# Kernel tuning notes

Hardware: AMD Instinct MI355X
Metric: run time of the kernel (lower is better)

The kernel has to match this reference:

```python
import jax, jax.numpy as jnp
import numpy as np

N = 50000; E = 200000; H = 128; L = 3; T = 2; FOUT = 64
G = 1000; NP = 3; ATOM_V = 64; BOND_V = 8
EPS = 1e-5
_DEG_HIST = np.array([0., 50000., 75000., 50000., 25000.])
# PyG PNAConv: avg_deg['log'] = sum(hist[d] * log(d+1)) / num_nodes
AVG_DEG_LOG = float((np.log(np.arange(5) + 1.0) * _DEG_HIST).sum() / _DEG_HIST.sum())


def _bn(v, g, b):
    # training-mode BatchNorm1d (biased variance), eps=1e-5
    mu = v.mean(0)
    var = ((v - mu) ** 2).mean(0)
    return (v - mu) * jax.lax.rsqrt(var + EPS) * g + b


def setup_inputs() -> dict:
    key = jax.random.key(0)
    ks = jax.random.split(key, 16)
    def nrm(k, shape, fan):
        return (jax.random.normal(k, shape, dtype=jnp.float32) / np.sqrt(fan)).astype(jnp.float32)
    return {
        'x': jax.random.randint(ks[0], (N, 9), 0, ATOM_V),
        'edge_index': jax.random.randint(ks[1], (2, E), 0, N),
        'batch': jnp.sort(jax.random.randint(ks[2], (N,), 0, G)),
        'edge_attr_idx': jax.random.randint(ks[3], (E, 3), 0, BOND_V),
        'atom_emb': nrm(ks[4], (9, ATOM_V, H), H),
        'bond_emb': nrm(ks[5], (3, BOND_V, H), H),
        'edge_W': nrm(ks[6], (L, H, H), H), 'edge_b': jnp.zeros((L, H), jnp.float32),
        'pre_W': nrm(ks[7], (L, T, 3 * H, H), 3 * H), 'pre_b': jnp.zeros((L, T, H), jnp.float32),
        'post_W': nrm(ks[8], (L, T, 13 * H, FOUT), 13 * H), 'post_b': jnp.zeros((L, T, FOUT), jnp.float32),
        'lin_W': nrm(ks[9], (L, H, H), H), 'lin_b': jnp.zeros((L, H), jnp.float32),
        'bn_g': jnp.ones((L, H), jnp.float32), 'bn_b': jnp.zeros((L, H), jnp.float32),
        'mlp_W': nrm(ks[10], (2, H, H), H), 'mlp_b': jnp.zeros((2, H), jnp.float32),
        'mlp_g': jnp.ones((2, H), jnp.float32), 'mlp_be': jnp.zeros((2, H), jnp.float32),
        'hW1': nrm(ks[11], (H, H // 2), H), 'hb1': jnp.zeros((H // 2,), jnp.float32),
        'hg1': jnp.ones((H // 2,), jnp.float32), 'hbe1': jnp.zeros((H // 2,), jnp.float32),
        'hW2': nrm(ks[12], (H // 2, H // 4), H // 2), 'hb2': jnp.zeros((H // 4,), jnp.float32),
        'hg2': jnp.ones((H // 4,), jnp.float32), 'hbe2': jnp.zeros((H // 4,), jnp.float32),
        'hW3': nrm(ks[13], (H // 4, NP), H // 4), 'hb3': jnp.zeros((NP,), jnp.float32),
    }


def reference(x, edge_index, batch, edge_attr_idx, atom_emb, bond_emb,
              edge_W, edge_b, pre_W, pre_b, post_W, post_b, lin_W, lin_b,
              bn_g, bn_b, mlp_W, mlp_b, mlp_g, mlp_be,
              hW1, hb1, hg1, hbe1, hW2, hb2, hg2, hbe2, hW3, hb3):
    # encoders: sum of per-feature embeddings (OGB Atom/Bond encoder)
    h = atom_emb[jnp.arange(9), x].sum(1)               # [N,H]
    e = bond_emb[jnp.arange(3), edge_attr_idx].sum(1)   # [E,H]
    src, dst = edge_index[0], edge_index[1]
    cnt = jax.ops.segment_sum(jnp.ones((E,), jnp.float32), dst, N)
    deg = jnp.maximum(cnt, 1.0)[:, None, None]          # clamp(1), as in PyG scalers
    amp = jnp.log(deg + 1.0) / AVG_DEG_LOG
    att = AVG_DEG_LOG / jnp.log(deg + 1.0)
    has = (cnt > 0)[:, None, None]
    for l in range(L):
        ea = e @ edge_W[l] + edge_b[l]                                  # [E,H]
        msg_in = jnp.concatenate([h[dst], h[src], ea], -1)              # [E,3H]
        m = jnp.einsum('ef,tfh->eth', msg_in, pre_W[l]) + pre_b[l]      # [E,T,H]
        s1 = jax.ops.segment_sum(m, dst, N)
        s2 = jax.ops.segment_sum(m * m, dst, N)
        mean = s1 / deg
        std = jnp.sqrt(jax.nn.relu(s2 / deg - mean * mean) + EPS)
        mn = jnp.where(has, jax.ops.segment_min(m, dst, N), 0.0)
        mx = jnp.where(has, jax.ops.segment_max(m, dst, N), 0.0)
        agg = jnp.concatenate([mean, mn, mx, std], -1)                  # [N,T,4H]
        scaled = jnp.concatenate([agg, agg * amp, agg * att], -1)       # [N,T,12H]
        upd = jnp.concatenate(
            [jnp.broadcast_to(h[:, None, :], (N, T, H)), scaled], -1)   # [N,T,13H]
        o = jnp.einsum('ntf,tfo->nto', upd, post_W[l]) + post_b[l]      # [N,T,FOUT]
        o = o.reshape(N, T * FOUT) @ lin_W[l] + lin_b[l]                # [N,H]
        h = jax.nn.relu(_bn(o, bn_g[l], bn_b[l]))
    g = jax.ops.segment_sum(h, batch, G)                                # [G,H]
    for i in range(2):
        g = jax.nn.relu(_bn(g @ mlp_W[i] + mlp_b[i], mlp_g[i], mlp_be[i]))
    g = jax.nn.relu(_bn(g @ hW1 + hb1, hg1, hbe1))
    g = jax.nn.relu(_bn(g @ hW2 + hb2, hg2, hbe2))
    return g @ hW3 + hb3                                                # [G,NP]
```

## Files before the change

### kernel.cpp

```cpp
#include <hip/hip_runtime.h>
#include <math.h>


#define NN 50000
#define NE 200000
#define HD 128
#define NG 1000
#define EPSV 1e-5f
#define ALOGC 1.1330197327247628f

#define AP 1288
#define OPF 132
#define ECAP 512
#define SCB 49

typedef __bf16 bf16x8 __attribute__((ext_vector_type(8)));
typedef float f32x4 __attribute__((ext_vector_type(4)));

__device__ __forceinline__ unsigned short f2bf(float f) {
    unsigned int u = __float_as_uint(f);
    unsigned int r = (u + 0x7FFFu + ((u >> 16) & 1u)) >> 16;
    return (unsigned short)r;
}
__device__ __forceinline__ float bf2f(unsigned short h) {
    return __uint_as_float((unsigned int)h << 16);
}

__global__ void k_fill(float* __restrict__ o, float v, int n) {
    int i = blockIdx.x * 256 + threadIdx.x;
    if (i < n) o[i] = v;
}

__global__ void k_zero(float* __restrict__ z, int n) {
    int i = blockIdx.x * 256 + threadIdx.x;
    if (i < n) z[i] = 0.f;
}

__global__ __launch_bounds__(256) void k_encode_nodes(
    const int* __restrict__ x, const float* __restrict__ aemb, float* __restrict__ h) {
    __shared__ int xi[8][9];
    int nb = blockIdx.x * 8;
    int tid = threadIdx.x;
    if (tid < 72) xi[tid / 9][tid % 9] = x[nb * 9 + tid];
    __syncthreads();
    int node = tid >> 5, c4 = (tid & 31) * 4;
    float4 acc = make_float4(0.f, 0.f, 0.f, 0.f);
#pragma unroll
    for (int f = 0; f < 9; ++f) {
        float4 e = *(const float4*)(aemb + (size_t)(f * 64 + xi[node][f]) * HD + c4);
        acc.x += e.x; acc.y += e.y; acc.z += e.z; acc.w += e.w;
    }
    *(float4*)(h + (size_t)(nb + node) * HD + c4) = acc;
}

__global__ void k_count(const int* __restrict__ dst, int* __restrict__ cnt) {
    int e = blockIdx.x * 256 + threadIdx.x;
    if (e < NE) atomicAdd(&cnt[dst[e]], 1);
}

__global__ __launch_bounds__(1024) void k_scanA(const int* __restrict__ cnt,
                                                int* __restrict__ sc, int* __restrict__ tot) {
    __shared__ int buf[1024];
    int tid = threadIdx.x;
    int i = blockIdx.x * 1024 + tid;
    int v = (i < NN) ? cnt[i] : 0;
    buf[tid] = v;
    __syncthreads();
    for (int s = 1; s < 1024; s <<= 1) {
        int t = (tid >= s) ? buf[tid - s] : 0;
        __syncthreads();
        buf[tid] += t;
        __syncthreads();
    }
    if (i < NN) sc[i] = buf[tid];
    if (tid == 1023) tot[blockIdx.x] = buf[1023];
}

__global__ void k_scanB(const int* __restrict__ tot, int* __restrict__ offb) {
    if (threadIdx.x == 0) {
        int run = 0;
        for (int b = 0; b < SCB; ++b) { offb[b] = run; run += tot[b]; }
    }
}

__global__ __launch_bounds__(1024) void k_scanC(
    const int* __restrict__ cnt, const int* __restrict__ sc, const int* __restrict__ offb,
    int* __restrict__ rowptr, float* __restrict__ ampv, float* __restrict__ attv) {
    int i = blockIdx.x * 1024 + threadIdx.x;
    if (i == 0) rowptr[0] = 0;
    if (i < NN) {
        rowptr[i + 1] = offb[blockIdx.x] + sc[i];
        int v = cnt[i];
        float dg = (float)(v > 0 ? v : 1);
        float lg = logf(dg + 1.0f);
        ampv[i] = lg / ALOGC;
        attv[i] = ALOGC / lg;
    }
}

__global__ void k_scatter(const int* __restrict__ dst, const int* __restrict__ rowptr,
                          int* __restrict__ fill, int* __restrict__ eperm) {
    int e = blockIdx.x * 256 + threadIdx.x;
    if (e < NE) {
        int d = dst[e];
        int pos = rowptr[d] + atomicAdd(&fill[d], 1);
        eperm[pos] = e;
    }
}

__global__ void k_eprep(const int* __restrict__ ei, const int* __restrict__ eai,
                        const int* __restrict__ eperm, int* __restrict__ precs) {
    int p = blockIdx.x * 256 + threadIdx.x;
    if (p < NE) {
        int e = eperm[p];
        int cidx = eai[e * 3] | (eai[e * 3 + 1] << 3) | (eai[e * 3 + 2] << 6);
        precs[p] = ei[e] | (cidx << 17);
    }
}

__global__ void k_fold(const float* __restrict__ edge_W, const float* __restrict__ edge_b,
                       const float* __restrict__ pre_W, const float* __restrict__ pre_b,
                       float* __restrict__ cW, float* __restrict__ tb) {
    int l = blockIdx.y;
    int k = blockIdx.x;
    int tj = threadIdx.x;
    int t = tj >> 7, j = tj & 127;
    const float* pw = pre_W + ((size_t)(l * 2 + t) * 384 + 256) * 128 + j;
    if (k < 128) {
        const float* ew = edge_W + ((size_t)l * 128 + k) * 128;
        float acc = 0.f;
        for (int i = 0; i < 128; ++i) acc += ew[i] * pw[i * 128];
        cW[((size_t)l * 128 + k) * 256 + tj] = acc;
    } else {
        const float* eb = edge_b + l * 128;
        float acc = pre_b[(l * 2 + t) * 128 + j];
        for (int i = 0; i < 128; ++i) acc += eb[i] * pw[i * 128];
        tb[l * 256 + tj] = acc;
    }
}

__global__ void k_bond(const float* __restrict__ bemb, const float* __restrict__ cW,
                       float* __restrict__ bondc) {
    int v = blockIdx.x, f = blockIdx.y, l = blockIdx.z;
    int tj = threadIdx.x;
    const float* src = bemb + (size_t)(f * 8 + v) * 128;
    const float* w = cW + (size_t)l * 128 * 256;
    float acc = 0.f;
    for (int i = 0; i < 128; ++i) acc += src[i] * w[i * 256 + tj];
    bondc[(((size_t)l * 3 + f) * 8 + v) * 256 + tj] = acc;
}

__global__ void k_bcomb(const float* __restrict__ bondc, unsigned short* __restrict__ bcomb) {
    int ci = blockIdx.x, l = blockIdx.y, tj = threadIdx.x;
    const float* base = bondc + (size_t)l * 3 * 8 * 256;
    float v = base[((0 * 8) + (ci & 7)) * 256 + tj]
            + base[((1 * 8) + ((ci >> 3) & 7)) * 256 + tj]
            + base[((2 * 8) + (ci >> 6)) * 256 + tj];
    bcomb[((size_t)l * 512 + ci) * 256 + tj] = f2bf(v);
}

__device__ __forceinline__ void pack_body2(const float* __restrict__ W, int N, int NT,
                                           unsigned short* __restrict__ pkh,
                                           unsigned short* __restrict__ pkl,
                                           int blk, int lane) {
    int kstep = blk / NT, nt = blk - kstep * NT;
    int kb = kstep * 32 + (lane >> 4) * 8;
    int col = nt * 16 + (lane & 15);
    unsigned short th[8], tl[8];
#pragma unroll
    for (int i = 0; i < 8; ++i) {
        float w = W[(size_t)(kb + i) * N + col];
        unsigned short hh = f2bf(w);
        th[i] = hh;
        tl[i] = f2bf(w - bf2f(hh));
    }
    size_t base = ((size_t)blk * 64 + lane) * 8;
    *(uint4*)(pkh + base) = *(uint4*)th;
    *(uint4*)(pkl + base) = *(uint4*)tl;
}

__global__ __launch_bounds__(64) void k_packall(
    const float* __restrict__ post_W, const float* __restrict__ lin_W,
    const float* __restrict__ pre_W,
    unsigned short* __restrict__ pkPostHi, unsigned short* __restrict__ pkPostLo,
    unsigned short* __restrict__ pkLinHi, unsigned short* __restrict__ pkLinLo,
    unsigned short* __restrict__ pkPreHi, unsigned short* __restrict__ pkPreLo) {
    int b = blockIdx.x;
    int lane = threadIdx.x;
    if (b < 1248) {
        int l = b / 416, rem = b % 416;
        int t = rem / 208, blk = rem % 208;
        size_t off = ((size_t)l * 2 + t) * 106496;
        pack_body2(post_W + ((size_t)l * 2 + t) * 1664 * 64, 64, 4,
                   pkPostHi + off, pkPostLo + off, blk, lane);
    } else if (b < 1344) {
        int idx = b - 1248;
        int l = idx / 32, blk = idx % 32;
        pack_body2(lin_W + (size_t)l * 128 * 128, 128, 8,
                   pkLinHi + (size_t)l * 16384, pkLinLo + (size_t)l * 16384, blk, lane);
    } else {
        int idx = b - 1344;
        int l = idx / 128, bb = idx % 128;
        const float* preW = pre_W + (size_t)l * 2 * 384 * 128;
        unsigned short* phi = pkPreHi + (size_t)l * 65536;
        unsigned short* plo = pkPreLo + (size_t)l * 65536;
        int kstep = bb >> 5, nt = bb & 31;
        int q = lane >> 4, nc = lane & 15;
        int col = nt * 16 + nc;
        int t = (col >> 7) & 1;
        int jcol = col & 127;
        int fbase = (col < 256) ? 0 : 128;
        unsigned short hi[8], lo[8];
#pragma unroll
        for (int i = 0; i < 8; ++i) {
            int k = kstep * 32 + q * 8 + i;
            float w = preW[((size_t)t * 384 + fbase + k) * 128 + jcol];
            unsigned short h16 = f2bf(w);
            hi[i] = h16;
            lo[i] = f2bf(w - bf2f(h16));
        }
        size_t base = ((size_t)bb * 64 + lane) * 8;
        *(uint4*)(phi + base) = *(uint4*)hi;
        *(uint4*)(plo + base) = *(uint4*)lo;
    }
}

__device__ __forceinline__ void pre_mfma_body(
    const unsigned short* __restrict__ ah, const unsigned short* __restrict__ al,
    const unsigned short* __restrict__ phi, const unsigned short* __restrict__ plo,
    const float* __restrict__ tb, int n0, int tid,
    float* __restrict__ hzd, unsigned short* __restrict__ hzs) {
    int lane = tid & 63, w = tid >> 6;
    int q = lane >> 4, nc = lane & 15;
    f32x4 acc[8];
#pragma unroll
    for (int j = 0; j < 8; ++j) acc[j] = (f32x4){0.f, 0.f, 0.f, 0.f};
#pragma unroll
    for (int kk = 0; kk < 4; ++kk) {
        bf16x8 Ahi = *(const bf16x8*)(ah + nc * 136 + kk * 32 + q * 8);
        bf16x8 Alo = *(const bf16x8*)(al + nc * 136 + kk * 32 + q * 8);
#pragma unroll
        for (int j = 0; j < 8; ++j) {
            int nt = w * 8 + j;
            size_t base = ((size_t)(kk * 32 + nt) * 64 + lane) * 8;
            bf16x8 Bhi = *(const bf16x8*)(phi + base);
            bf16x8 Blo = *(const bf16x8*)(plo + base);
            acc[j] = __builtin_amdgcn_mfma_f32_16x16x32_bf16(Ahi, Bhi, acc[j], 0, 0, 0);
            acc[j] = __builtin_amdgcn_mfma_f32_16x16x32_bf16(Ahi, Blo, acc[j], 0, 0, 0);
            acc[j] = __builtin_amdgcn_mfma_f32_16x16x32_bf16(Alo, Bhi, acc[j], 0, 0, 0);
        }
    }
#pragma unroll
    for (int j = 0; j < 8; ++j) {
        int col = (w * 8 + j) * 16 + nc;
#pragma unroll
        for (int reg = 0; reg < 4; ++reg) {
            int row = n0 + q * 4 + reg;
            if (col < 256) hzd[(size_t)row * 256 + col] = acc[j][reg] + tb[col];
            else           hzs[(size_t)row * 256 + (col - 256)] = f2bf(acc[j][reg]);
        }
    }
}

__global__ __launch_bounds__(256) void k_pre_m(
    const float* __restrict__ h,
    const unsigned short* __restrict__ phi, const unsigned short* __restrict__ plo,
    const float* __restrict__ tb,
    float* __restrict__ hzd, unsigned short* __restrict__ hzs) {
    __shared__ __align__(16) unsigned short ah[16 * 136];
    __shared__ __align__(16) unsigned short al[16 * 136];
    int n0 = blockIdx.x * 16;
    int tid = threadIdx.x;
    {
        int node = tid >> 4, cg = (tid & 15) * 8;
        const float* hs = h + (size_t)(n0 + node) * HD + cg;
        float4 v0 = *(const float4*)(hs);
        float4 v1 = *(const float4*)(hs + 4);
        float vv[8] = {v0.x, v0.y, v0.z, v0.w, v1.x, v1.y, v1.z, v1.w};
        unsigned short hh[8], ll[8];
#pragma unroll
        for (int i = 0; i < 8; ++i) {
            hh[i] = f2bf(vv[i]);
            ll[i] = f2bf(vv[i] - bf2f(hh[i]));
        }
        *(uint4*)(ah + node * 136 + cg) = *(uint4*)hh;
        *(uint4*)(al + node * 136 + cg) = *(uint4*)ll;
    }
    __syncthreads();
    pre_mfma_body(ah, al, phi, plo, tb, n0, tid, hzd, hzs);
}

__global__ __launch_bounds__(256) void k_bnpre(
    const float* __restrict__ o2, const float* __restrict__ stats,
    const float* __restrict__ g, const float* __restrict__ b,
    const unsigned short* __restrict__ phi, const unsigned short* __restrict__ plo,
    const float* __restrict__ tb,
    float* __restrict__ h, float* __restrict__ hzd, unsigned short* __restrict__ hzs) {
    __shared__ __align__(16) unsigned short ah[16 * 136];
    __shared__ __align__(16) unsigned short al[16 * 136];
    int n0 = blockIdx.x * 16;
    int tid = threadIdx.x;
    {
        int node = tid >> 4, cg = (tid & 15) * 8;
        int n = n0 + node;
        const float* os = o2 + (size_t)n * HD + cg;
        float4 v0 = *(const float4*)(os);
        float4 v1 = *(const float4*)(os + 4);
        float vv[8] = {v0.x, v0.y, v0.z, v0.w, v1.x, v1.y, v1.z, v1.w};
        unsigned short hh[8], ll[8];
        float ou[8];
#pragma unroll
        for (int i = 0; i < 8; ++i) {
            int c = cg + i;
            float mu = stats[c] * (1.f / NN);
            float var = stats[128 + c] * (1.f / NN) - mu * mu;
            float val = (vv[i] - mu) * rsqrtf(var + EPSV) * g[c] + b[c];
            val = fmaxf(val, 0.f);
            ou[i] = val;
            hh[i] = f2bf(val);
            ll[i] = f2bf(val - bf2f(hh[i]));
        }
        float* hd = h + (size_t)n * HD + cg;
        *(float4*)(hd) = make_float4(ou[0], ou[1], ou[2], ou[3]);
        *(float4*)(hd + 4) = make_float4(ou[4], ou[5], ou[6], ou[7]);
        *(uint4*)(ah + node * 136 + cg) = *(uint4*)hh;
        *(uint4*)(al + node * 136 + cg) = *(uint4*)ll;
    }
    __syncthreads();
    pre_mfma_body(ah, al, phi, plo, tb, n0, tid, hzd, hzs);
}

__global__ __launch_bounds__(256) void k_post(
    const float* __restrict__ h,
    const float* __restrict__ hzd, const unsigned short* __restrict__ hzs,
    const int* __restrict__ rowptr, const int* __restrict__ precs,
    const unsigned short* __restrict__ bcomb,
    const float* __restrict__ ampv, const float* __restrict__ attv,
    const unsigned short* __restrict__ pkPostHi, const unsigned short* __restrict__ pkPostLo,
    const float* __restrict__ postb,
    const unsigned short* __restrict__ pkLinHi, const unsigned short* __restrict__ pkLinLo,
    const float* __restrict__ linb,
    float* __restrict__ o2, float* __restrict__ stats) {
    __shared__ __align__(16) unsigned short a_lds[16 * AP];
    __shared__ __align__(16) float o_f[16 * OPF];
    __shared__ int es[ECAP];
    __shared__ float s_amp[16], s_att[16];
    int n0 = blockIdx.x * 16;
    int tid = threadIdx.x;

    int pbase = rowptr[n0];
    int ecount = rowptr[n0 + 16] - pbase;
    for (int i = tid; i < ecount && i < ECAP; i += 256) es[i] = precs[pbase + i];
    {
        int node = tid >> 4, cg = (tid & 15) * 8;
        const float* hs = h + (size_t)(n0 + node) * HD + cg;
        float4 v0 = *(const float4*)(hs);
        float4 v1 = *(const float4*)(hs + 4);
        unsigned short* d0 = a_lds + node * AP + cg;
        unsigned short* d1 = d0 + 640;
        unsigned short bb[8];
        bb[0] = f2bf(v0.x); bb[1] = f2bf(v0.y); bb[2] = f2bf(v0.z); bb[3] = f2bf(v0.w);
        bb[4] = f2bf(v1.x); bb[5] = f2bf(v1.y); bb[6] = f2bf(v1.z); bb[7] = f2bf(v1.w);
#pragma unroll
        for (int i = 0; i < 8; ++i) { d0[i] = bb[i]; d1[i] = bb[i]; }
    }
    if (tid < 16) { s_amp[tid] = ampv[n0 + tid]; s_att[tid] = attv[n0 + tid]; }
    __syncthreads();

    {
        int wv = tid >> 6, lane = tid & 63;
        int cc = lane * 4;
        int tt = cc >> 7, jj = cc & 127;
        bool incap = (ecount <= ECAP);
        const float4 Z4 = make_float4(0.f, 0.f, 0.f, 0.f);
        const float4 BIG = make_float4(3.4e38f, 3.4e38f, 3.4e38f, 3.4e38f);
        const float4 NBIG = make_float4(-3.4e38f, -3.4e38f, -3.4e38f, -3.4e38f);

#define EDGE_ACC(P, S1, S2, MN, MX)                                                       \
        {                                                                                 \
            int rec = incap ? es[(P) - pbase] : precs[(P)];                               \
            int sp = rec & 131071;                                                        \
            int ci = rec >> 17;                                                           \
            uint2 uv = *(const uint2*)(hzs + (size_t)sp * 256 + cc);                      \
            uint2 ub = *(const uint2*)(bcomb + (size_t)ci * 256 + cc);                    \
            float wx = __uint_as_float(uv.x << 16) + __uint_as_float(ub.x << 16);         \
            float wy = __uint_as_float(uv.x & 0xffff0000u) + __uint_as_float(ub.x & 0xffff0000u); \
            float wz = __uint_as_float(uv.y << 16) + __uint_as_float(ub.y << 16);         \
            float ww = __uint_as_float(uv.y & 0xffff0000u) + __uint_as_float(ub.y & 0xffff0000u); \
            S1.x += wx; S1.y += wy; S1.z += wz; S1.w += ww;                               \
            S2.x += wx * wx; S2.y += wy * wy; S2.z += wz * wz; S2.w += ww * ww;           \
            MN.x = fminf(MN.x, wx); MN.y = fminf(MN.y, wy);                               \
            MN.z = fminf(MN.z, wz); MN.w = fminf(MN.w, ww);                               \
            MX.x = fmaxf(MX.x, wx); MX.y = fmaxf(MX.y, wy);                               \
            MX.z = fmaxf(MX.z, wz); MX.w = fmaxf(MX.w, ww);                               \
        }

        auto fin = [&](int r, int cnt, float4 hd, float4 s1, float4 s2, float4 mn, float4 mx) {
            float inv = 1.f / (float)(cnt > 0 ? cnt : 1);
            float4 mw, stdv, mean;
            mw.x = s1.x * inv; mw.y = s1.y * inv; mw.z = s1.z * inv; mw.w = s1.w * inv;
            stdv.x = sqrtf(fmaxf(s2.x * inv - mw.x * mw.x, 0.f) + EPSV);
            stdv.y = sqrtf(fmaxf(s2.y * inv - mw.y * mw.y, 0.f) + EPSV);
            stdv.z = sqrtf(fmaxf(s2.z * inv - mw.z * mw.z, 0.f) + EPSV);
            stdv.w = sqrtf(fmaxf(s2.w * inv - mw.w * mw.w, 0.f) + EPSV);
            if (cnt > 0) {
                mean.x = hd.x + mw.x; mean.y = hd.y + mw.y;
                mean.z = hd.z + mw.z; mean.w = hd.w + mw.w;
                mn.x += hd.x; mn.y += hd.y; mn.z += hd.z; mn.w += hd.w;
                mx.x += hd.x; mx.y += hd.y; mx.z += hd.z; mx.w += hd.w;
            } else {
                mean = Z4; mn = Z4; mx = Z4;
            }
            unsigned short* d = a_lds + r * AP + tt * 640 + 128 + jj;
            d[0] = f2bf(mean.x); d[1] = f2bf(mean.y); d[2] = f2bf(mean.z); d[3] = f2bf(mean.w);
            d += 128; d[0] = f2bf(mn.x); d[1] = f2bf(mn.y); d[2] = f2bf(mn.z); d[3] = f2bf(mn.w);
            d += 128; d[0] = f2bf(mx.x); d[1] = f2bf(mx.y); d[2] = f2bf(mx.z); d[3] = f2bf(mx.w);
            d += 128; d[0] = f2bf(stdv.x); d[1] = f2bf(stdv.y); d[2] = f2bf(stdv.z); d[3] = f2bf(stdv.w);
        };

        for (int i = 0; i < 2; ++i) {
            int ra = wv * 4 + i * 2;
            int rb = ra + 1;
            int na = n0 + ra, nb = n0 + rb;
            int pa0 = rowptr[na], pa1 = rowptr[na + 1];
            int pb0 = rowptr[nb], pb1 = rowptr[nb + 1];
            float4 hda = *(const float4*)(hzd + (size_t)na * 256 + cc);
            float4 hdb = *(const float4*)(hzd + (size_t)nb * 256 + cc);
            float4 s1a = Z4, s2a = Z4, mna = BIG, mxa = NBIG;
            float4 s1b = Z4, s2b = Z4, mnb = BIG, mxb = NBIG;
            int da = pa1 - pa0, db = pb1 - pb0;
            int mc = (da < db) ? da : db;
            for (int k = 0; k < mc; ++k) {
                EDGE_ACC(pa0 + k, s1a, s2a, mna, mxa)
                EDGE_ACC(pb0 + k, s1b, s2b, mnb, mxb)
            }
            for (int k = mc; k < da; ++k) EDGE_ACC(pa0 + k, s1a, s2a, mna, mxa)
            for (int k = mc; k < db; ++k) EDGE_ACC(pb0 + k, s1b, s2b, mnb, mxb)
            fin(ra, da, hda, s1a, s2a, mna, mxa);
            fin(rb, db, hdb, s1b, s2b, mnb, mxb);
        }
#undef EDGE_ACC
    }
    __syncthreads();

    {
        int lane = tid & 63;
        int w = tid >> 6;
        int t = w >> 1;
        int ntb = (w & 1) * 2;
        int q = lane >> 4, nc = lane & 15;
        const unsigned short* arow = a_lds + (size_t)nc * AP + t * 640 + q * 8;
        size_t toff = (size_t)t * 106496;
        const unsigned short* pkh = pkPostHi + toff;
        const unsigned short* pkl = pkPostLo + toff;
        f32x4 aP0 = {0.f, 0.f, 0.f, 0.f}, aP1 = {0.f, 0.f, 0.f, 0.f};
        f32x4 aA0 = {0.f, 0.f, 0.f, 0.f}, aA1 = {0.f, 0.f, 0.f, 0.f};
        f32x4 aT0 = {0.f, 0.f, 0.f, 0.f}, aT1 = {0.f, 0.f, 0.f, 0.f};
        for (int kk = 0; kk < 20; ++kk) {
            bf16x8 af = *(const bf16x8*)(arow + kk * 32);
            size_t ib = ((size_t)(kk * 4 + ntb) * 64 + lane) * 8;
            aP0 = __builtin_amdgcn_mfma_f32_16x16x32_bf16(af, *(const bf16x8*)(pkh + ib), aP0, 0, 0, 0);
            aP0 = __builtin_amdgcn_mfma_f32_16x16x32_bf16(af, *(const bf16x8*)(pkl + ib), aP0, 0, 0, 0);
            aP1 = __builtin_amdgcn_mfma_f32_16x16x32_bf16(af, *(const bf16x8*)(pkh + ib + 512), aP1, 0, 0, 0);
            aP1 = __builtin_amdgcn_mfma_f32_16x16x32_bf16(af, *(const bf16x8*)(pkl + ib + 512), aP1, 0, 0, 0);
            if (kk >= 4) {
                size_t ia = ((size_t)((kk + 16) * 4 + ntb) * 64 + lane) * 8;
                aA0 = __builtin_amdgcn_mfma_f32_16x16x32_bf16(af, *(const bf16x8*)(pkh + ia), aA0, 0, 0, 0);
                aA0 = __builtin_amdgcn_mfma_f32_16x16x32_bf16(af, *(const bf16x8*)(pkl + ia), aA0, 0, 0, 0);
                aA1 = __builtin_amdgcn_mfma_f32_16x16x32_bf16(af, *(const bf16x8*)(pkh + ia + 512), aA1, 0, 0, 0);
                aA1 = __builtin_amdgcn_mfma_f32_16x16x32_bf16(af, *(const bf16x8*)(pkl + ia + 512), aA1, 0, 0, 0);
                size_t it = ((size_t)((kk + 32) * 4 + ntb) * 64 + lane) * 8;
                aT0 = __builtin_amdgcn_mfma_f32_16x16x32_bf16(af, *(const bf16x8*)(pkh + it), aT0, 0, 0, 0);
                aT0 = __builtin_amdgcn_mfma_f32_16x16x32_bf16(af, *(const bf16x8*)(pkl + it), aT0, 0, 0, 0);
                aT1 = __builtin_amdgcn_mfma_f32_16x16x32_bf16(af, *(const bf16x8*)(pkh + it + 512), aT1, 0, 0, 0);
                aT1 = __builtin_amdgcn_mfma_f32_16x16x32_bf16(af, *(const bf16x8*)(pkl + it + 512), aT1, 0, 0, 0);
            }
        }
#pragma unroll
        for (int u = 0; u < 2; ++u) {
            int nt = ntb + u;
            int col = t * 64 + nt * 16 + nc;
            float pbia = postb[t * 64 + nt * 16 + nc];
            f32x4 P = u ? aP1 : aP0;
            f32x4 A = u ? aA1 : aA0;
            f32x4 T = u ? aT1 : aT0;
#pragma unroll
            for (int reg = 0; reg < 4; ++reg) {
                int mrow = q * 4 + reg;
                o_f[mrow * OPF + col] = P[reg] + s_amp[mrow] * A[reg] + s_att[mrow] * T[reg] + pbia;
            }
        }
    }
    __syncthreads();

    {
        int lane = tid & 63;
        int w = tid >> 6;
        int ntb = w * 2;
        int q = lane >> 4, nc = lane & 15;
        const float* arow = o_f + (size_t)nc * OPF + q * 8;
        f32x4 L0 = {0.f, 0.f, 0.f, 0.f}, L1 = {0.f, 0.f, 0.f, 0.f};
#pragma unroll
        for (int kk = 0; kk < 4; ++kk) {
            float4 a0 = *(const float4*)(arow + kk * 32);
            float4 a1 = *(const float4*)(arow + kk * 32 + 4);
            float vv[8] = {a0.x, a0.y, a0.z, a0.w, a1.x, a1.y, a1.z, a1.w};
            unsigned short hh[8], ll[8];
#pragma unroll
            for (int i = 0; i < 8; ++i) {
                hh[i] = f2bf(vv[i]);
                ll[i] = f2bf(vv[i] - bf2f(hh[i]));
            }
            bf16x8 Ahi = *(const bf16x8*)hh;
            bf16x8 Alo = *(const bf16x8*)ll;
            size_t ib = ((size_t)(kk * 8 + ntb) * 64 + lane) * 8;
            bf16x8 B0h = *(const bf16x8*)(pkLinHi + ib);
            bf16x8 B0l = *(const bf16x8*)(pkLinLo + ib);
            bf16x8 B1h = *(const bf16x8*)(pkLinHi + ib + 512);
            bf16x8 B1l = *(const bf16x8*)(pkLinLo + ib + 512);
            L0 = __builtin_amdgcn_mfma_f32_16x16x32_bf16(Ahi, B0h, L0, 0, 0, 0);
            L0 = __builtin_amdgcn_mfma_f32_16x16x32_bf16(Alo, B0h, L0, 0, 0, 0);
            L0 = __builtin_amdgcn_mfma_f32_16x16x32_bf16(Ahi, B0l, L0, 0, 0, 0);
            L1 = __builtin_amdgcn_mfma_f32_16x16x32_bf16(Ahi, B1h, L1, 0, 0, 0);
            L1 = __builtin_amdgcn_mfma_f32_16x16x32_bf16(Alo, B1h, L1, 0, 0, 0);
            L1 = __builtin_amdgcn_mfma_f32_16x16x32_bf16(Ahi, B1l, L1, 0, 0, 0);
        }
#pragma unroll
        for (int u = 0; u < 2; ++u) {
            int col = (ntb + u) * 16 + nc;
            float lb = linb[col];
            f32x4 L = u ? L1 : L0;
            float ps = 0.f, pss = 0.f;
#pragma unroll
            for (int reg = 0; reg < 4; ++reg) {
                int mrow = q * 4 + reg;
                float v = L[reg] + lb;
                o2[(size_t)(n0 + mrow) * HD + col] = v;
                ps += v; pss += v * v;
            }
            ps += __shfl_down(ps, 16); ps += __shfl_down(ps, 32);
            pss += __shfl_down(pss, 16); pss += __shfl_down(pss, 32);
            if (q == 0) {
                atomicAdd(&stats[col], ps);
                atomicAdd(&stats[128 + col], pss);
            }
        }
    }
}

__global__ void k_bn_relu(const float* __restrict__ o2, const float* __restrict__ stats,
                          const float* __restrict__ g, const float* __restrict__ b,
                          float* __restrict__ h) {
    int idx = blockIdx.x * 256 + threadIdx.x;
    int c = idx & 127;
    float mu = stats[c] * (1.f / NN);
    float var = stats[128 + c] * (1.f / NN) - mu * mu;
    float v = (o2[idx] - mu) * rsqrtf(var + EPSV) * g[c] + b[c];
    h[idx] = fmaxf(v, 0.f);
}

__global__ void k_pool(const float* __restrict__ h, const int* __restrict__ batch,
                       float* __restrict__ g0) {
    int c = threadIdx.x;
    int nbase = blockIdx.x * 64;
    float run = 0.f; int cur = -1;
    for (int i = 0; i < 64; ++i) {
        int n = nbase + i;
        if (n >= NN) break;
        int bb = batch[n];
        if (bb != cur) {
            if (cur >= 0) atomicAdd(&g0[(size_t)cur * HD + c], run);
            cur = bb; run = 0.f;
        }
        run += h[(size_t)n * HD + c];
    }
    if (cur >= 0) atomicAdd(&g0[(size_t)cur * HD + c], run);
}

__global__ void k_head_gemm(const float* __restrict__ x, const float* __restrict__ W,
                            const float* __restrict__ b, float* __restrict__ y,
                            float* __restrict__ stats, int K, int Kout) {
    int row = blockIdx.x;
    int col = threadIdx.x;
    if (col >= Kout) return;
    float acc = b[col];
    for (int k = 0; k < K; k += 4) {
        float4 xv = *(const float4*)(x + (size_t)row * K + k);
        acc += xv.x * W[(k + 0) * Kout + col] + xv.y * W[(k + 1) * Kout + col]
             + xv.z * W[(k + 2) * Kout + col] + xv.w * W[(k + 3) * Kout + col];
    }
    y[(size_t)row * Kout + col] = acc;
    if (stats) {
        atomicAdd(&stats[col], acc);
        atomicAdd(&stats[Kout + col], acc * acc);
    }
}

__global__ __launch_bounds__(128) void k_head_fused(
    const float* __restrict__ y_in, const float* __restrict__ stats_in,
    const float* __restrict__ g, const float* __restrict__ b,
    const float* __restrict__ W, const float* __restrict__ bias,
    float* __restrict__ y_out, float* __restrict__ stats_out, int Kin, int Kout) {
    __shared__ float row[128];
    int r = blockIdx.x, tid = threadIdx.x;
    if (tid < Kin) {
        float mu = stats_in[tid] * (1.f / NG);
        float var = stats_in[Kin + tid] * (1.f / NG) - mu * mu;
        float v = (y_in[(size_t)r * Kin + tid] - mu) * rsqrtf(var + EPSV) * g[tid] + b[tid];
        row[tid] = fmaxf(v, 0.f);
    }
    __syncthreads();
    if (tid < Kout) {
        float acc = bias[tid];
        for (int k = 0; k < Kin; ++k) acc += row[k] * W[(size_t)k * Kout + tid];
        y_out[(size_t)r * Kout + tid] = acc;
        if (stats_out) {
            atomicAdd(&stats_out[tid], acc);
            atomicAdd(&stats_out[Kout + tid], acc * acc);
        }
    }
}

extern "C" void kernel_launch(void* const* d_in, const int* in_sizes, int n_in,
                              void* d_out, int out_size, void* d_ws, size_t ws_size,
                              hipStream_t stream) {
    const int*   x        = (const int*)  d_in[0];
    const int*   ei       = (const int*)  d_in[1];
    const int*   batch    = (const int*)  d_in[2];
    const int*   eai      = (const int*)  d_in[3];
    const float* atom_emb = (const float*)d_in[4];
    const float* bond_emb = (const float*)d_in[5];
    const float* edge_W   = (const float*)d_in[6];
    const float* edge_b   = (const float*)d_in[7];
    const float* pre_W    = (const float*)d_in[8];
    const float* pre_b    = (const float*)d_in[9];
    const float* post_W   = (const float*)d_in[10];
    const float* post_b   = (const float*)d_in[11];
    const float* lin_W    = (const float*)d_in[12];
    const float* lin_b    = (const float*)d_in[13];
    const float* bn_g     = (const float*)d_in[14];
    const float* bn_b     = (const float*)d_in[15];
    const float* mlp_W    = (const float*)d_in[16];
    const float* mlp_b    = (const float*)d_in[17];
    const float* mlp_g    = (const float*)d_in[18];
    const float* mlp_be   = (const float*)d_in[19];
    const float* hW1 = (const float*)d_in[20]; const float* hb1  = (const float*)d_in[21];
    const float* hg1 = (const float*)d_in[22]; const float* hbe1 = (const float*)d_in[23];
    const float* hW2 = (const float*)d_in[24]; const float* hb2  = (const float*)d_in[25];
    const float* hg2 = (const float*)d_in[26]; const float* hbe2 = (const float*)d_in[27];
    const float* hW3 = (const float*)d_in[28]; const float* hb3  = (const float*)d_in[29];
    float* out = (float*)d_out;
    (void)n_in; (void)in_sizes;

    char* p = (char*)d_ws;
    size_t off = 0;
    auto alloc = [&](size_t bytes) -> char* {
        char* r = p + off;
        off += (bytes + 255) & ~(size_t)255;
        return r;
    };
    float* h     = (float*)alloc((size_t)NN * HD * 4);
    float* o2    = (float*)alloc((size_t)NN * HD * 4);
    float* hzd   = (float*)alloc((size_t)NN * 256 * 4);
    unsigned short* hzs = (unsigned short*)alloc((size_t)NN * 256 * 2);
    float* ampv  = (float*)alloc((size_t)NN * 4);
    float* attv  = (float*)alloc((size_t)NN * 4);
    int*   rowptr= (int*)  alloc((size_t)(NN + 1) * 4);
    int*   eperm = (int*)  alloc((size_t)NE * 4);
    int*   precs = (int*)  alloc((size_t)NE * 4);
    int*   sc    = (int*)  alloc((size_t)NN * 4);
    int*   stot  = (int*)  alloc((size_t)SCB * 4);
    int*   soff  = (int*)  alloc((size_t)SCB * 4);
    float* cW    = (float*)alloc((size_t)3 * 128 * 256 * 4);
    float* tbb   = (float*)alloc((size_t)3 * 256 * 4);
    float* bondc = (float*)alloc((size_t)3 * 3 * 8 * 256 * 4);
    unsigned short* bcomb = (unsigned short*)alloc((size_t)3 * 512 * 256 * 2);
    unsigned short* pkPostHi = (unsigned short*)alloc((size_t)3 * 2 * 106496 * 2);
    unsigned short* pkPostLo = (unsigned short*)alloc((size_t)3 * 2 * 106496 * 2);
    unsigned short* pkLinHi  = (unsigned short*)alloc((size_t)3 * 16384 * 2);
    unsigned short* pkLinLo  = (unsigned short*)alloc((size_t)3 * 16384 * 2);
    unsigned short* pkPreHi  = (unsigned short*)alloc((size_t)3 * 65536 * 2);
    unsigned short* pkPreLo  = (unsigned short*)alloc((size_t)3 * 65536 * 2);
    float* gA    = (float*)alloc((size_t)NG * HD * 4);
    float* gB    = (float*)alloc((size_t)NG * HD * 4);
    char* z0 = p + off;
    int*   cnt   = (int*)  alloc((size_t)NN * 4);
    int*   fill  = (int*)  alloc((size_t)NN * 4);
    float* stats = (float*)alloc((size_t)3 * 256 * 4);
    float* hstats= (float*)alloc((size_t)4 * 256 * 4);
    float* g0    = (float*)alloc((size_t)NG * HD * 4);
    size_t zwords = (size_t)((p + off) - z0) / 4;

    if (off > ws_size) {
        k_fill<<<(out_size + 255) / 256, 256, 0, stream>>>(out, (float)ws_size, out_size);
        return;
    }

    k_zero<<<(int)((zwords + 255) / 256), 256, 0, stream>>>((float*)z0, (int)zwords);
    k_encode_nodes<<<NN / 8, 256, 0, stream>>>(x, atom_emb, h);
    k_count<<<(NE + 255) / 256, 256, 0, stream>>>(ei + NE, cnt);
    k_scanA<<<SCB, 1024, 0, stream>>>(cnt, sc, stot);
    k_scanB<<<1, 64, 0, stream>>>(stot, soff);
    k_scanC<<<SCB, 1024, 0, stream>>>(cnt, sc, soff, rowptr, ampv, attv);
    k_scatter<<<(NE + 255) / 256, 256, 0, stream>>>(ei + NE, rowptr, fill, eperm);
    k_eprep<<<(NE + 255) / 256, 256, 0, stream>>>(ei, eai, eperm, precs);
    k_fold<<<dim3(129, 3), 256, 0, stream>>>(edge_W, edge_b, pre_W, pre_b, cW, tbb);
    k_bond<<<dim3(8, 3, 3), 256, 0, stream>>>(bond_emb, cW, bondc);
    k_bcomb<<<dim3(512, 3), 256, 0, stream>>>(bondc, bcomb);
    k_packall<<<1728, 64, 0, stream>>>(post_W, lin_W, pre_W,
        pkPostHi, pkPostLo, pkLinHi, pkLinLo, pkPreHi, pkPreLo);

    for (int l = 0; l < 3; ++l) {
        if (l == 0) {
            k_pre_m<<<NN / 16, 256, 0, stream>>>(h, pkPreHi, pkPreLo, tbb, hzd, hzs);
        } else {
            k_bnpre<<<NN / 16, 256, 0, stream>>>(o2, stats + (l - 1) * 256,
                bn_g + (l - 1) * 128, bn_b + (l - 1) * 128,
                pkPreHi + (size_t)l * 65536, pkPreLo + (size_t)l * 65536,
                tbb + l * 256, h, hzd, hzs);
        }
        k_post<<<NN / 16, 256, 0, stream>>>(h, hzd, hzs, rowptr, precs,
            bcomb + (size_t)l * 512 * 256,
            ampv, attv,
            pkPostHi + (size_t)l * 2 * 106496, pkPostLo + (size_t)l * 2 * 106496,
            post_b + l * 2 * 64,
            pkLinHi + (size_t)l * 16384, pkLinLo + (size_t)l * 16384,
            lin_b + l * 128,
            o2, stats + l * 256);
    }
    k_bn_relu<<<(NN * HD) / 256, 256, 0, stream>>>(o2, stats + 2 * 256,
        bn_g + 2 * 128, bn_b + 2 * 128, h);

    k_pool<<<(NN + 63) / 64, 128, 0, stream>>>(h, batch, g0);

    k_head_gemm<<<NG, 128, 0, stream>>>(g0, mlp_W, mlp_b, gA, hstats, 128, 128);
    k_head_fused<<<NG, 128, 0, stream>>>(gA, hstats, mlp_g, mlp_be,
        mlp_W + 128 * 128, mlp_b + 128, gB, hstats + 256, 128, 128);
    k_head_fused<<<NG, 128, 0, stream>>>(gB, hstats + 256, mlp_g + 128, mlp_be + 128,
        hW1, hb1, gA, hstats + 512, 128, 64);
    k_head_fused<<<NG, 128, 0, stream>>>(gA, hstats + 512, hg1, hbe1,
        hW2, hb2, gB, hstats + 768, 64, 32);
    k_head_fused<<<NG, 128, 0, stream>>>(gB, hstats + 768, hg2, hbe2,
        hW3, hb3, out, (float*)nullptr, 32, 3);
}
```

Before: 939.2 us.

## Fuse prep kernels, store hzd in bf16, fold final BN-ReLU into pooling

Several unrelated changes at once. The edge-scatter and edge-prep kernels are merged so packed edge records are written straight to their sorted position, and the bond-projection and bond-combine kernels become one kernel. The final BN+ReLU is folded into the graph pooling kernel. The per-node destination projection hzd is stored as bf16 instead of fp32, which halves its memory traffic in k_post at some cost in precision. The LDS staging of edge records in k_post is removed, so records are now read directly from global memory.

Result: no change. 946.7 us (+0.8%).

```diff
diff --git a/kernel.cpp b/kernel.cpp
--- a/kernel.cpp
+++ b/kernel.cpp
@@ -11,7 +11,6 @@
 
 #define AP 1288
 #define OPF 132
-#define ECAP 512
 #define SCB 49
 
 typedef __bf16 bf16x8 __attribute__((ext_vector_type(8)));
@@ -98,23 +97,15 @@
     }
 }
 
-__global__ void k_scatter(const int* __restrict__ dst, const int* __restrict__ rowptr,
-                          int* __restrict__ fill, int* __restrict__ eperm) {
+__global__ void k_scatter(const int* __restrict__ ei, const int* __restrict__ eai,
+                          const int* __restrict__ rowptr,
+                          int* __restrict__ fill, int* __restrict__ precs) {
     int e = blockIdx.x * 256 + threadIdx.x;
     if (e < NE) {
-        int d = dst[e];
+        int d = ei[NE + e];
         int pos = rowptr[d] + atomicAdd(&fill[d], 1);
-        eperm[pos] = e;
-    }
-}
-
-__global__ void k_eprep(const int* __restrict__ ei, const int* __restrict__ eai,
-                        const int* __restrict__ eperm, int* __restrict__ precs) {
-    int p = blockIdx.x * 256 + threadIdx.x;
-    if (p < NE) {
-        int e = eperm[p];
         int cidx = eai[e * 3] | (eai[e * 3 + 1] << 3) | (eai[e * 3 + 2] << 6);
-        precs[p] = ei[e] | (cidx << 17);
+        precs[pos] = ei[e] | (cidx << 17);
     }
 }
 
@@ -139,24 +130,16 @@
     }
 }
 
-__global__ void k_bond(const float* __restrict__ bemb, const float* __restrict__ cW,
-                       float* __restrict__ bondc) {
-    int v = blockIdx.x, f = blockIdx.y, l = blockIdx.z;
-    int tj = threadIdx.x;
-    const float* src = bemb + (size_t)(f * 8 + v) * 128;
+__global__ void k_bcomb2(const float* __restrict__ bemb, const float* __restrict__ cW,
+                         unsigned short* __restrict__ bcomb) {
+    int ci = blockIdx.x, l = blockIdx.y, tj = threadIdx.x;
+    const float* s0 = bemb + (size_t)(0 * 8 + (ci & 7)) * 128;
+    const float* s1 = bemb + (size_t)(1 * 8 + ((ci >> 3) & 7)) * 128;
+    const float* s2 = bemb + (size_t)(2 * 8 + (ci >> 6)) * 128;
     const float* w = cW + (size_t)l * 128 * 256;
     float acc = 0.f;
-    for (int i = 0; i < 128; ++i) acc += src[i] * w[i * 256 + tj];
-    bondc[(((size_t)l * 3 + f) * 8 + v) * 256 + tj] = acc;
-}
-
-__global__ void k_bcomb(const float* __restrict__ bondc, unsigned short* __restrict__ bcomb) {
-    int ci = blockIdx.x, l = blockIdx.y, tj = threadIdx.x;
-    const float* base = bondc + (size_t)l * 3 * 8 * 256;
-    float v = base[((0 * 8) + (ci & 7)) * 256 + tj]
-            + base[((1 * 8) + ((ci >> 3) & 7)) * 256 + tj]
-            + base[((2 * 8) + (ci >> 6)) * 256 + tj];
-    bcomb[((size_t)l * 512 + ci) * 256 + tj] = f2bf(v);
+    for (int i = 0; i < 128; ++i) acc += (s0[i] + s1[i] + s2[i]) * w[i * 256 + tj];
+    bcomb[((size_t)l * 512 + ci) * 256 + tj] = f2bf(acc);
 }
 
 __device__ __forceinline__ void pack_body2(const float* __restrict__ W, int N, int NT,
@@ -229,7 +212,7 @@
     const unsigned short* __restrict__ ah, const unsigned short* __restrict__ al,
     const unsigned short* __restrict__ phi, const unsigned short* __restrict__ plo,
     const float* __restrict__ tb, int n0, int tid,
-    float* __restrict__ hzd, unsigned short* __restrict__ hzs) {
+    unsigned short* __restrict__ hzd, unsigned short* __restrict__ hzs) {
     int lane = tid & 63, w = tid >> 6;
     int q = lane >> 4, nc = lane & 15;
     f32x4 acc[8];
@@ -256,7 +239,7 @@
 #pragma unroll
         for (int reg = 0; reg < 4; ++reg) {
             int row = n0 + q * 4 + reg;
-            if (col < 256) hzd[(size_t)row * 256 + col] = acc[j][reg] + tb[col];
+            if (col < 256) hzd[(size_t)row * 256 + col] = f2bf(acc[j][reg] + tb[col]);
             else           hzs[(size_t)row * 256 + (col - 256)] = f2bf(acc[j][reg]);
         }
     }
@@ -266,7 +249,7 @@
     const float* __restrict__ h,
     const unsigned short* __restrict__ phi, const unsigned short* __restrict__ plo,
     const float* __restrict__ tb,
-    float* __restrict__ hzd, unsigned short* __restrict__ hzs) {
+    unsigned short* __restrict__ hzd, unsigned short* __restrict__ hzs) {
     __shared__ __align__(16) unsigned short ah[16 * 136];
     __shared__ __align__(16) unsigned short al[16 * 136];
     int n0 = blockIdx.x * 16;
@@ -295,7 +278,7 @@
     const float* __restrict__ g, const float* __restrict__ b,
     const unsigned short* __restrict__ phi, const unsigned short* __restrict__ plo,
     const float* __restrict__ tb,
-    float* __restrict__ h, float* __restrict__ hzd, unsigned short* __restrict__ hzs) {
+    float* __restrict__ h, unsigned short* __restrict__ hzd, unsigned short* __restrict__ hzs) {
     __shared__ __align__(16) unsigned short ah[16 * 136];
     __shared__ __align__(16) unsigned short al[16 * 136];
     int n0 = blockIdx.x * 16;
@@ -332,7 +315,7 @@
 
 __global__ __launch_bounds__(256) void k_post(
     const float* __restrict__ h,
-    const float* __restrict__ hzd, const unsigned short* __restrict__ hzs,
+    const unsigned short* __restrict__ hzd, const unsigned short* __restrict__ hzs,
     const int* __restrict__ rowptr, const int* __restrict__ precs,
     const unsigned short* __restrict__ bcomb,
     const float* __restrict__ ampv, const float* __restrict__ attv,
@@ -343,14 +326,10 @@
     float* __restrict__ o2, float* __restrict__ stats) {
     __shared__ __align__(16) unsigned short a_lds[16 * AP];
     __shared__ __align__(16) float o_f[16 * OPF];
-    __shared__ int es[ECAP];
     __shared__ float s_amp[16], s_att[16];
     int n0 = blockIdx.x * 16;
     int tid = threadIdx.x;
 
-    int pbase = rowptr[n0];
-    int ecount = rowptr[n0 + 16] - pbase;
-    for (int i = tid; i < ecount && i < ECAP; i += 256) es[i] = precs[pbase + i];
     {
         int node = tid >> 4, cg = (tid & 15) * 8;
         const float* hs = h + (size_t)(n0 + node) * HD + cg;
@@ -371,14 +350,13 @@
         int wv = tid >> 6, lane = tid & 63;
         int cc = lane * 4;
         int tt = cc >> 7, jj = cc & 127;
-        bool incap = (ecount <= ECAP);
         const float4 Z4 = make_float4(0.f, 0.f, 0.f, 0.f);
         const float4 BIG = make_float4(3.4e38f, 3.4e38f, 3.4e38f, 3.4e38f);
         const float4 NBIG = make_float4(-3.4e38f, -3.4e38f, -3.4e38f, -3.4e38f);
 
 #define EDGE_ACC(P, S1, S2, MN, MX)                                                       \
         {                                                                                 \
-            int rec = incap ? es[(P) - pbase] : precs[(P)];                               \
+            int rec = precs[(P)];                                                         \
             int sp = rec & 131071;                                                        \
             int ci = rec >> 17;                                                           \
             uint2 uv = *(const uint2*)(hzs + (size_t)sp * 256 + cc);                      \
@@ -424,8 +402,13 @@
             int na = n0 + ra, nb = n0 + rb;
             int pa0 = rowptr[na], pa1 = rowptr[na + 1];
             int pb0 = rowptr[nb], pb1 = rowptr[nb + 1];
-            float4 hda = *(const float4*)(hzd + (size_t)na * 256 + cc);
-            float4 hdb = *(const float4*)(hzd + (size_t)nb * 256 + cc);
+            uint2 uda = *(const uint2*)(hzd + (size_t)na * 256 + cc);
+            uint2 udb = *(const uint2*)(hzd + (size_t)nb * 256 + cc);
+            float4 hda, hdb;
+            hda.x = __uint_as_float(uda.x << 16); hda.y = __uint_as_float(uda.x & 0xffff0000u);
+            hda.z = __uint_as_float(uda.y << 16); hda.w = __uint_as_float(uda.y & 0xffff0000u);
+            hdb.x = __uint_as_float(udb.x << 16); hdb.y = __uint_as_float(udb.x & 0xffff0000u);
+            hdb.z = __uint_as_float(udb.y << 16); hdb.w = __uint_as_float(udb.y & 0xffff0000u);
             float4 s1a = Z4, s2a = Z4, mna = BIG, mxa = NBIG;
             float4 s1b = Z4, s2b = Z4, mnb = BIG, mxb = NBIG;
             int da = pa1 - pa0, db = pb1 - pb0;
@@ -548,31 +531,25 @@
     }
 }
 
-__global__ void k_bn_relu(const float* __restrict__ o2, const float* __restrict__ stats,
-                          const float* __restrict__ g, const float* __restrict__ b,
-                          float* __restrict__ h) {
-    int idx = blockIdx.x * 256 + threadIdx.x;
-    int c = idx & 127;
+__global__ void k_pool(const float* __restrict__ o2, const float* __restrict__ stats,
+                       const float* __restrict__ g, const float* __restrict__ b,
+                       const int* __restrict__ batch, float* __restrict__ g0) {
+    int c = threadIdx.x;
     float mu = stats[c] * (1.f / NN);
     float var = stats[128 + c] * (1.f / NN) - mu * mu;
-    float v = (o2[idx] - mu) * rsqrtf(var + EPSV) * g[c] + b[c];
-    h[idx] = fmaxf(v, 0.f);
-}
-
-__global__ void k_pool(const float* __restrict__ h, const int* __restrict__ batch,
-                       float* __restrict__ g0) {
-    int c = threadIdx.x;
+    float rs = rsqrtf(var + EPSV) * g[c];
+    float bb = b[c];
     int nbase = blockIdx.x * 64;
     float run = 0.f; int cur = -1;
     for (int i = 0; i < 64; ++i) {
         int n = nbase + i;
         if (n >= NN) break;
-        int bb = batch[n];
-        if (bb != cur) {
+        int bi = batch[n];
+        if (bi != cur) {
             if (cur >= 0) atomicAdd(&g0[(size_t)cur * HD + c], run);
-            cur = bb; run = 0.f;
-        }
-        run += h[(size_t)n * HD + c];
+            cur = bi; run = 0.f;
+        }
+        run += fmaxf((o2[(size_t)n * HD + c] - mu) * rs + bb, 0.f);
     }
     if (cur >= 0) atomicAdd(&g0[(size_t)cur * HD + c], run);
 }
@@ -661,19 +638,17 @@
     };
     float* h     = (float*)alloc((size_t)NN * HD * 4);
     float* o2    = (float*)alloc((size_t)NN * HD * 4);
-    float* hzd   = (float*)alloc((size_t)NN * 256 * 4);
+    unsigned short* hzd = (unsigned short*)alloc((size_t)NN * 256 * 2);
     unsigned short* hzs = (unsigned short*)alloc((size_t)NN * 256 * 2);
     float* ampv  = (float*)alloc((size_t)NN * 4);
     float* attv  = (float*)alloc((size_t)NN * 4);
     int*   rowptr= (int*)  alloc((size_t)(NN + 1) * 4);
-    int*   eperm = (int*)  alloc((size_t)NE * 4);
     int*   precs = (int*)  alloc((size_t)NE * 4);
     int*   sc    = (int*)  alloc((size_t)NN * 4);
     int*   stot  = (int*)  alloc((size_t)SCB * 4);
     int*   soff  = (int*)  alloc((size_t)SCB * 4);
     float* cW    = (float*)alloc((size_t)3 * 128 * 256 * 4);
     float* tbb   = (float*)alloc((size_t)3 * 256 * 4);
-    float* bondc = (float*)alloc((size_t)3 * 3 * 8 * 256 * 4);
     unsigned short* bcomb = (unsigned short*)alloc((size_t)3 * 512 * 256 * 2);
     unsigned short* pkPostHi = (unsigned short*)alloc((size_t)3 * 2 * 106496 * 2);
     unsigned short* pkPostLo = (unsigned short*)alloc((size_t)3 * 2 * 106496 * 2);
@@ -702,11 +677,9 @@
     k_scanA<<<SCB, 1024, 0, stream>>>(cnt, sc, stot);
     k_scanB<<<1, 64, 0, stream>>>(stot, soff);
     k_scanC<<<SCB, 1024, 0, stream>>>(cnt, sc, soff, rowptr, ampv, attv);
-    k_scatter<<<(NE + 255) / 256, 256, 0, stream>>>(ei + NE, rowptr, fill, eperm);
-    k_eprep<<<(NE + 255) / 256, 256, 0, stream>>>(ei, eai, eperm, precs);
+    k_scatter<<<(NE + 255) / 256, 256, 0, stream>>>(ei, eai, rowptr, fill, precs);
     k_fold<<<dim3(129, 3), 256, 0, stream>>>(edge_W, edge_b, pre_W, pre_b, cW, tbb);
-    k_bond<<<dim3(8, 3, 3), 256, 0, stream>>>(bond_emb, cW, bondc);
-    k_bcomb<<<dim3(512, 3), 256, 0, stream>>>(bondc, bcomb);
+    k_bcomb2<<<dim3(512, 3), 256, 0, stream>>>(bond_emb, cW, bcomb);
     k_packall<<<1728, 64, 0, stream>>>(post_W, lin_W, pre_W,
         pkPostHi, pkPostLo, pkLinHi, pkLinLo, pkPreHi, pkPreLo);
 
@@ -728,10 +701,9 @@
             lin_b + l * 128,
             o2, stats + l * 256);
     }
-    k_bn_relu<<<(NN * HD) / 256, 256, 0, stream>>>(o2, stats + 2 * 256,
-        bn_g + 2 * 128, bn_b + 2 * 128, h);
-
-    k_pool<<<(NN + 63) / 64, 128, 0, stream>>>(h, batch, g0);
+
+    k_pool<<<(NN + 63) / 64, 128, 0, stream>>>(o2, stats + 2 * 256,
+        bn_g + 2 * 128, bn_b + 2 * 128, batch, g0);
 
     k_head_gemm<<<NG, 128, 0, stream>>>(g0, mlp_W, mlp_b, gA, hstats, 128, 128);
     k_head_fused<<<NG, 128, 0, stream>>>(gA, hstats, mlp_g, mlp_be,
```
